# Kernel tuning notes

Hardware: AMD Instinct MI355X
Metric: run time of the kernel (lower is better)

## Reference

```python
import jax, jax.numpy as jnp
import numpy as np

SCALE = 0.5
DROP_P = 0.2

def setup_inputs() -> dict:
    key = jax.random.key(0)
    k1, k2 = jax.random.split(key)
    x1 = jax.random.normal(k1, (8, 2048, 128), dtype=jnp.float32)
    x2 = jax.random.normal(k2, (8, 2048, 128), dtype=jnp.float32)
    return {"x1": x1, "x2": x2}

def reference(x1, x2):
    # scores: [B, M, N] = x1 @ x2^T, scaled by 0.5
    scores = jnp.einsum('bmd,bnd->bmn', x1, x2) * SCALE
    probs = jax.nn.softmax(scores, axis=-1)
    # dropout p=0.2 (training mode in the torch source); fixed key for determinism
    keep = jax.random.bernoulli(jax.random.key(42), 1.0 - DROP_P, probs.shape)
    probs = jnp.where(keep, probs / (1.0 - DROP_P), 0.0)
    # out: [B, M, D] = probs @ x2
    return jnp.einsum('bmn,bnd->bmd', probs, x2)
```

## Files before the change

### kernel.cpp

```cpp
#include <hip/hip_runtime.h>
#include <stdint.h>


typedef __bf16 bf16x8 __attribute__((ext_vector_type(8)));
typedef float f32x4 __attribute__((ext_vector_type(4)));

union FragAB {
  bf16x8 v;
  uint32_t u[4];
};

__device__ __forceinline__ uint32_t rotl32(uint32_t x, uint32_t r) {
  return (x << r) | (x >> (32u - r));
}

__device__ __forceinline__ void threefry2x32_k42(uint32_t in0, uint32_t in1,
                                                 uint32_t& o0, uint32_t& o1) {
  const uint32_t ks0 = 0u;
  const uint32_t ks1 = 42u;
  const uint32_t ks2 = 0x1BD11BDAu ^ 0u ^ 42u;
  uint32_t x0 = in0 + ks0;
  uint32_t x1 = in1 + ks1;
#define TFR(r) { x0 += x1; x1 = rotl32(x1, r); x1 ^= x0; }
  TFR(13u) TFR(15u) TFR(26u) TFR(6u)
  x0 += ks1; x1 += ks2 + 1u;
  TFR(17u) TFR(29u) TFR(16u) TFR(24u)
  x0 += ks2; x1 += ks0 + 2u;
  TFR(13u) TFR(15u) TFR(26u) TFR(6u)
  x0 += ks0; x1 += ks1 + 3u;
  TFR(17u) TFR(29u) TFR(16u) TFR(24u)
  x0 += ks1; x1 += ks2 + 4u;
  TFR(13u) TFR(15u) TFR(26u) TFR(6u)
  x0 += ks2; x1 += ks0 + 5u;
#undef TFR
  o0 = x0; o1 = x1;
}

__device__ __forceinline__ uint32_t pack_bf16(float a, float b) {
  __bf16 ba = (__bf16)a;
  __bf16 bb = (__bf16)b;
  uint32_t ua = (uint32_t)__builtin_bit_cast(uint16_t, ba);
  uint32_t ub = (uint32_t)__builtin_bit_cast(uint16_t, bb);
  return ua | (ub << 16);
}

#define KEEP_LT 3435974144u
#define MBIAS 40.0f

__launch_bounds__(256, 4)
__global__ void prep_kernel(const float* __restrict__ x2,
                            uint4* __restrict__ KF,
                            uint4* __restrict__ VF) {
  const int tid = threadIdx.x;
  const int w = tid >> 6;
  const int lane = tid & 63;
  const int l15 = lane & 15;
  const int g = lane >> 4;
  const int T = blockIdx.x;
  const int b = blockIdx.y;
  const float* xb = x2 + (size_t)b * 2048 * 128;

  #pragma unroll
  for (int h = 0; h < 2; ++h) {
    const int n = T * 32 + h * 16 + l15;
    const float* p = xb + (size_t)n * 128 + w * 32 + 8 * g;
    float4 f0 = *(const float4*)(p);
    float4 f1 = *(const float4*)(p + 4);
    uint4 u;
    u.x = pack_bf16(f0.x, f0.y);
    u.y = pack_bf16(f0.z, f0.w);
    u.z = pack_bf16(f1.x, f1.y);
    u.w = pack_bf16(f1.z, f1.w);
    KF[(size_t)((b * 64 + T) * 8 + w * 2 + h) * 64 + lane] = u;
  }

  #pragma unroll
  for (int i = 0; i < 2; ++i) {
    const int dt = w + 4 * i;
    const int d = dt * 16 + l15;
    const float* p = xb + (size_t)(T * 32 + 8 * g) * 128 + d;
    uint4 u;
    u.x = pack_bf16(p[0],   p[128]);
    u.y = pack_bf16(p[256], p[384]);
    u.z = pack_bf16(p[512], p[640]);
    u.w = pack_bf16(p[768], p[896]);
    VF[(size_t)((b * 64 + T) * 8 + dt) * 64 + lane] = u;
  }
}

__launch_bounds__(256, 4)
__global__ void attn2_kernel(const float* __restrict__ x1,
                             const uint4* __restrict__ KF,
                             const uint4* __restrict__ VF,
                             float* __restrict__ out) {
  __shared__ __attribute__((aligned(16))) uint32_t SMEM[8768];

  const int tid = threadIdx.x;
  const int w = __builtin_amdgcn_readfirstlane(tid >> 6);
  const int lane = tid & 63;
  const int l15 = lane & 15;
  const int g = lane >> 4;
  const int b = blockIdx.y;
  const int m0 = blockIdx.x * 16;

  uint32_t* PbW = &SMEM[w * 320];

  const float QSCALE = 0.5f * 1.44269504088896340736f;
  FragAB qf[4];
  {
    const float* qp_base = x1 + ((size_t)b * 2048 + m0 + l15) * 128;
    #pragma unroll
    for (int c = 0; c < 4; ++c) {
      const float* qp = qp_base + c * 32 + g * 8;
      float4 f0 = *(const float4*)(qp);
      float4 f1 = *(const float4*)(qp + 4);
      qf[c].u[0] = pack_bf16(f0.x * QSCALE, f0.y * QSCALE);
      qf[c].u[1] = pack_bf16(f0.z * QSCALE, f0.w * QSCALE);
      qf[c].u[2] = pack_bf16(f1.x * QSCALE, f1.y * QSCALE);
      qf[c].u[3] = pack_bf16(f1.z * QSCALE, f1.w * QSCALE);
    }
  }

  f32x4 o[8];
  #pragma unroll
  for (int dt = 0; dt < 8; ++dt) o[dt] = (f32x4){0.f, 0.f, 0.f, 0.f};
  float lsum = 0.f;

  const uint32_t rb = (uint32_t)b * 4194304u +
                      (uint32_t)(m0 + l15) * 2048u + (uint32_t)(w * 512);

  const uint4* kfp = KF + (size_t)((b * 64 + w * 16) * 8) * 64 + lane;
  const uint4* vfp = VF + (size_t)((b * 64 + w * 16) * 8) * 64 + lane;

  for (int tile = 0; tile < 16; ++tile) {
    f32x4 sa[2];
    sa[0] = (f32x4){0.f, 0.f, 0.f, 0.f};
    sa[1] = (f32x4){0.f, 0.f, 0.f, 0.f};
    #pragma unroll
    for (int c = 0; c < 4; ++c) {
      uint4 a0 = kfp[(c * 2 + 0) * 64];
      uint4 a1 = kfp[(c * 2 + 1) * 64];
      FragAB k0, k1;
      k0.u[0] = a0.x; k0.u[1] = a0.y; k0.u[2] = a0.z; k0.u[3] = a0.w;
      k1.u[0] = a1.x; k1.u[1] = a1.y; k1.u[2] = a1.z; k1.u[3] = a1.w;
      sa[0] = __builtin_amdgcn_mfma_f32_16x16x32_bf16(k0.v, qf[c].v, sa[0], 0, 0, 0);
      sa[1] = __builtin_amdgcn_mfma_f32_16x16x32_bf16(k1.v, qf[c].v, sa[1], 0, 0, 0);
    }

    #pragma unroll
    for (int t = 0; t < 2; ++t) {
      float p0 = __builtin_amdgcn_exp2f(sa[t][0] - MBIAS);
      float p1 = __builtin_amdgcn_exp2f(sa[t][1] - MBIAS);
      float p2 = __builtin_amdgcn_exp2f(sa[t][2] - MBIAS);
      float p3 = __builtin_amdgcn_exp2f(sa[t][3] - MBIAS);
      lsum += (p0 + p1) + (p2 + p3);
      uint32_t ib = rb + (uint32_t)(tile * 32 + t * 16 + 4 * g);
      uint32_t h0, h1, bits;
      threefry2x32_k42(0u, ib + 0u, h0, h1); bits = h0 ^ h1;
      float q0 = (bits < KEEP_LT) ? p0 : 0.0f;
      threefry2x32_k42(0u, ib + 1u, h0, h1); bits = h0 ^ h1;
      float q1 = (bits < KEEP_LT) ? p1 : 0.0f;
      threefry2x32_k42(0u, ib + 2u, h0, h1); bits = h0 ^ h1;
      float q2 = (bits < KEEP_LT) ? p2 : 0.0f;
      threefry2x32_k42(0u, ib + 3u, h0, h1); bits = h0 ^ h1;
      float q3 = (bits < KEEP_LT) ? p3 : 0.0f;
      *(uint2*)&PbW[l15 * 20 + t * 8 + 2 * g] =
          make_uint2(pack_bf16(q0, q1), pack_bf16(q2, q3));
    }
    asm volatile("s_waitcnt lgkmcnt(0)" ::: "memory");
    FragAB pa;
    {
      uint4 pu = *(const uint4*)&PbW[l15 * 20 + 4 * g];
      pa.u[0] = pu.x; pa.u[1] = pu.y; pa.u[2] = pu.z; pa.u[3] = pu.w;
    }

    #pragma unroll
    for (int dt = 0; dt < 8; ++dt) {
      uint4 vv = vfp[dt * 64];
      FragAB vb;
      vb.u[0] = vv.x; vb.u[1] = vv.y; vb.u[2] = vv.z; vb.u[3] = vv.w;
      o[dt] = __builtin_amdgcn_mfma_f32_16x16x32_bf16(pa.v, vb.v, o[dt], 0, 0, 0);
    }
    kfp += 512;
    vfp += 512;
  }

  __syncthreads();
  float* EP = (float*)&SMEM[0];
  float* EPL = EP + 8192;
  EPL[l15 * 36 + w * 4 + g] = lsum;
  #pragma unroll
  for (int dt = 0; dt < 8; ++dt)
    #pragma unroll
    for (int r = 0; r < 4; ++r)
      EP[((w * 8 + dt) * 4 + r) * 64 + lane] = o[dt][r];
  __syncthreads();
  float scale[4];
  #pragma unroll
  for (int r = 0; r < 4; ++r) {
    const float4* lp = (const float4*)&EPL[(4 * g + r) * 36];
    float4 A = lp[0], B4 = lp[1], C4 = lp[2], D4 = lp[3];
    float L = ((A.x + A.y) + (A.z + A.w)) + ((B4.x + B4.y) + (B4.z + B4.w)) +
              ((C4.x + C4.y) + (C4.z + C4.w)) + ((D4.x + D4.y) + (D4.z + D4.w));
    scale[r] = 1.0f / (L * 0.8f);
  }
  #pragma unroll
  for (int i = 0; i < 2; ++i) {
    const int dt = w * 2 + i;
    #pragma unroll
    for (int r = 0; r < 4; ++r) {
      int base = (dt * 4 + r) * 64 + lane;
      float tot = EP[base] + EP[base + 2048] + EP[base + 4096] + EP[base + 6144];
      out[((size_t)b * 2048 + m0 + 4 * g + r) * 128 + dt * 16 + l15] =
          tot * scale[r];
    }
  }
}

__launch_bounds__(256, 2)
__global__ void attn_kernel(const float* __restrict__ x1,
                            const float* __restrict__ x2,
                            float* __restrict__ out) {
  __shared__ __attribute__((aligned(16))) uint32_t SMEM[4][4800];

  const int tid = threadIdx.x;
  const int wv = __builtin_amdgcn_readfirstlane(tid >> 6);
  const int lane = tid & 63;
  const int l15 = lane & 15;
  const int g = lane >> 4;
  const int b = blockIdx.y;
  const int m0 = blockIdx.x * 32;

  uint32_t* KtW = &SMEM[wv][0];
  uint32_t* VtW = &SMEM[wv][2176];
  uint32_t* PbW = &SMEM[wv][4480];

  const float QSCALE = 0.5f * 1.44269504088896340736f;
  FragAB qf[2][4];
  #pragma unroll
  for (int s = 0; s < 2; ++s) {
    const float* qp_base = x1 + ((size_t)b * 2048 + m0 + s * 16 + l15) * 128;
    #pragma unroll
    for (int c = 0; c < 4; ++c) {
      const float* qp = qp_base + c * 32 + g * 8;
      float4 f0 = *(const float4*)(qp);
      float4 f1 = *(const float4*)(qp + 4);
      qf[s][c].u[0] = pack_bf16(f0.x * QSCALE, f0.y * QSCALE);
      qf[s][c].u[1] = pack_bf16(f0.z * QSCALE, f0.w * QSCALE);
      qf[s][c].u[2] = pack_bf16(f1.x * QSCALE, f1.y * QSCALE);
      qf[s][c].u[3] = pack_bf16(f1.z * QSCALE, f1.w * QSCALE);
    }
  }

  f32x4 o[2][8];
  #pragma unroll
  for (int s = 0; s < 2; ++s)
    #pragma unroll
    for (int dt = 0; dt < 8; ++dt) o[s][dt] = (f32x4){0.f, 0.f, 0.f, 0.f};
  float lsum[2] = {0.f, 0.f};

  uint32_t rb[2];
  #pragma unroll
  for (int s = 0; s < 2; ++s)
    rb[s] = (uint32_t)b * 4194304u +
            (uint32_t)(m0 + s * 16 + l15) * 2048u + (uint32_t)(wv * 512);

  const float4* x2b4 = (const float4*)(x2 + (size_t)b * 2048 * 128);
  const uint32_t permsel = (l15 & 1) ? 0x07060302u : 0x05040100u;

  for (int tile = 0; tile < 16; ++tile) {
    const int n0g = wv * 512 + tile * 32;

    #pragma unroll
    for (int i = 0; i < 16; ++i) {
      int n = 2 * i + (lane >> 5);
      int dq = lane & 31;
      float4 v = x2b4[(size_t)(n0g + n) * 32 + dq];
      uint32_t p0 = pack_bf16(v.x, v.y);
      uint32_t p1 = pack_bf16(v.z, v.w);
      *(uint2*)&KtW[n * 68 + 2 * dq] = make_uint2(p0, p1);
      VtW[dq * 36 + n] = p0;
      VtW[(dq + 32) * 36 + n] = p1;
    }
    asm volatile("s_waitcnt lgkmcnt(0)" ::: "memory");

    f32x4 sa[2][2];
    #pragma unroll
    for (int s = 0; s < 2; ++s)
      #pragma unroll
      for (int t = 0; t < 2; ++t) sa[s][t] = (f32x4){0.f, 0.f, 0.f, 0.f};
    #pragma unroll
    for (int c = 0; c < 4; ++c) {
      FragAB k0, k1;
      uint4 a0 = *(const uint4*)&KtW[l15 * 68 + c * 16 + 4 * g];
      uint4 a1 = *(const uint4*)&KtW[(16 + l15) * 68 + c * 16 + 4 * g];
      k0.u[0] = a0.x; k0.u[1] = a0.y; k0.u[2] = a0.z; k0.u[3] = a0.w;
      k1.u[0] = a1.x; k1.u[1] = a1.y; k1.u[2] = a1.z; k1.u[3] = a1.w;
      sa[0][0] = __builtin_amdgcn_mfma_f32_16x16x32_bf16(k0.v, qf[0][c].v, sa[0][0], 0, 0, 0);
      sa[0][1] = __builtin_amdgcn_mfma_f32_16x16x32_bf16(k1.v, qf[0][c].v, sa[0][1], 0, 0, 0);
      sa[1][0] = __builtin_amdgcn_mfma_f32_16x16x32_bf16(k0.v, qf[1][c].v, sa[1][0], 0, 0, 0);
      sa[1][1] = __builtin_amdgcn_mfma_f32_16x16x32_bf16(k1.v, qf[1][c].v, sa[1][1], 0, 0, 0);
    }

    FragAB pa[2];
    #pragma unroll
    for (int s = 0; s < 2; ++s) {
      #pragma unroll
      for (int t = 0; t < 2; ++t) {
        float p0 = __builtin_amdgcn_exp2f(sa[s][t][0] - MBIAS);
        float p1 = __builtin_amdgcn_exp2f(sa[s][t][1] - MBIAS);
        float p2 = __builtin_amdgcn_exp2f(sa[s][t][2] - MBIAS);
        float p3 = __builtin_amdgcn_exp2f(sa[s][t][3] - MBIAS);
        lsum[s] += (p0 + p1) + (p2 + p3);
        uint32_t ib = rb[s] + (uint32_t)(tile * 32 + t * 16 + 4 * g);
        uint32_t h0, h1, bits;
        threefry2x32_k42(0u, ib + 0u, h0, h1); bits = h0 ^ h1;
        float q0 = (bits < KEEP_LT) ? p0 : 0.0f;
        threefry2x32_k42(0u, ib + 1u, h0, h1); bits = h0 ^ h1;
        float q1 = (bits < KEEP_LT) ? p1 : 0.0f;
        threefry2x32_k42(0u, ib + 2u, h0, h1); bits = h0 ^ h1;
        float q2 = (bits < KEEP_LT) ? p2 : 0.0f;
        threefry2x32_k42(0u, ib + 3u, h0, h1); bits = h0 ^ h1;
        float q3 = (bits < KEEP_LT) ? p3 : 0.0f;
        *(uint2*)&PbW[l15 * 20 + t * 8 + 2 * g] =
            make_uint2(pack_bf16(q0, q1), pack_bf16(q2, q3));
      }
      asm volatile("s_waitcnt lgkmcnt(0)" ::: "memory");
      uint4 pu = *(const uint4*)&PbW[l15 * 20 + 4 * g];
      pa[s].u[0] = pu.x; pa[s].u[1] = pu.y; pa[s].u[2] = pu.z; pa[s].u[3] = pu.w;
    }

    #pragma unroll
    for (int dt = 0; dt < 8; ++dt) {
      int rowp = ((l15 >> 1) & 1) * 32 + 4 * dt + (l15 >> 2);
      const uint32_t* vr = &VtW[rowp * 36 + 8 * g];
      uint4 U0 = *(const uint4*)vr;
      uint4 U1 = *(const uint4*)(vr + 4);
      FragAB vb;
      vb.u[0] = __builtin_amdgcn_perm(U0.y, U0.x, permsel);
      vb.u[1] = __builtin_amdgcn_perm(U0.w, U0.z, permsel);
      vb.u[2] = __builtin_amdgcn_perm(U1.y, U1.x, permsel);
      vb.u[3] = __builtin_amdgcn_perm(U1.w, U1.z, permsel);
      o[0][dt] = __builtin_amdgcn_mfma_f32_16x16x32_bf16(pa[0].v, vb.v, o[0][dt], 0, 0, 0);
      o[1][dt] = __builtin_amdgcn_mfma_f32_16x16x32_bf16(pa[1].v, vb.v, o[1][dt], 0, 0, 0);
    }
  }

  __syncthreads();
  float* EP = (float*)&SMEM[0][0];
  #pragma unroll
  for (int s = 0; s < 2; ++s) {
    #pragma unroll
    for (int dt = 0; dt < 8; ++dt)
      #pragma unroll
      for (int r = 0; r < 4; ++r)
        EP[(((wv * 2 + s) * 8 + dt) * 4 + r) * 64 + lane] = o[s][dt][r];
    EP[16384 + (s * 16 + l15) * 16 + wv * 4 + g] = lsum[s];
  }
  __syncthreads();
  const int s = wv >> 1;
  float scale[4];
  #pragma unroll
  for (int r = 0; r < 4; ++r) {
    const float4* lp = (const float4*)&EP[16384 + (s * 16 + 4 * g + r) * 16];
    float4 A = lp[0], B4 = lp[1], C4 = lp[2], D4 = lp[3];
    float L = ((A.x + A.y) + (A.z + A.w)) + ((B4.x + B4.y) + (B4.z + B4.w)) +
              ((C4.x + C4.y) + (C4.z + C4.w)) + ((D4.x + D4.y) + (D4.z + D4.w));
    scale[r] = 1.0f / (L * 0.8f);
  }
  #pragma unroll
  for (int it = 0; it < 4; ++it) {
    int dt = (wv * 4 + it) & 7;
    #pragma unroll
    for (int r = 0; r < 4; ++r) {
      int base = ((s * 8 + dt) * 4 + r) * 64 + lane;
      float tot = EP[base] + EP[base + 4096] + EP[base + 8192] + EP[base + 12288];
      out[((size_t)b * 2048 + m0 + s * 16 + 4 * g + r) * 128 + dt * 16 + l15] =
          tot * scale[r];
    }
  }
}

extern "C" void kernel_launch(void* const* d_in, const int* in_sizes, int n_in,
                              void* d_out, int out_size, void* d_ws, size_t ws_size,
                              hipStream_t stream) {
  const float* x1 = (const float*)d_in[0];
  const float* x2 = (const float*)d_in[1];
  float* out = (float*)d_out;
  if (d_ws != nullptr && ws_size >= (size_t)8 * 1024 * 1024) {
    uint4* KF = (uint4*)d_ws;
    uint4* VF = KF + 262144;
    prep_kernel<<<dim3(64, 8, 1), dim3(256, 1, 1), 0, stream>>>(x2, KF, VF);
    attn2_kernel<<<dim3(128, 8, 1), dim3(256, 1, 1), 0, stream>>>(x1, KF, VF, out);
  } else {
    attn_kernel<<<dim3(64, 8, 1), dim3(256, 1, 1), 0, stream>>>(x1, x2, out);
  }
}
```

Measured before the change: 146.1 us.

## Use 512-thread blocks sharing K/V tiles across two query halves

Replaces the 256-thread attention kernel with a 512-thread version where two groups of four waves handle two 16-row query slices that read the same K/V chunks. A per-tile barrier keeps them in lockstep so the shared K/V loads can hit in cache. Other changes: Q fragments now live in LDS instead of registers, block IDs are remapped so batch varies fastest, MFMA sections are wrapped in s_setprio, and the MBIAS subtraction before exp2 is dropped. Risks are the per-tile barrier stalls, extra LDS reads for Q, and possible exp overflow without the bias.

```diff
diff --git a/kernel.cpp b/kernel.cpp
--- a/kernel.cpp
+++ b/kernel.cpp
@@ -4,11 +4,6 @@
 
 typedef __bf16 bf16x8 __attribute__((ext_vector_type(8)));
 typedef float f32x4 __attribute__((ext_vector_type(4)));
-
-union FragAB {
-  bf16x8 v;
-  uint32_t u[4];
-};
 
 __device__ __forceinline__ uint32_t rotl32(uint32_t x, uint32_t r) {
   return (x << r) | (x >> (32u - r));
@@ -88,73 +83,83 @@
   }
 }
 
-__launch_bounds__(256, 4)
-__global__ void attn2_kernel(const float* __restrict__ x1,
+__launch_bounds__(512, 4)
+__global__ void attn6_kernel(const float* __restrict__ x1,
                              const uint4* __restrict__ KF,
                              const uint4* __restrict__ VF,
                              float* __restrict__ out) {
-  __shared__ __attribute__((aligned(16))) uint32_t SMEM[8768];
+  __shared__ __attribute__((aligned(16))) uint32_t SMEM[8832];
 
   const int tid = threadIdx.x;
   const int w = __builtin_amdgcn_readfirstlane(tid >> 6);
   const int lane = tid & 63;
   const int l15 = lane & 15;
   const int g = lane >> 4;
-  const int b = blockIdx.y;
-  const int m0 = blockIdx.x * 16;
-
-  uint32_t* PbW = &SMEM[w * 320];
+  const int q = w & 3;
+  const int hs = w >> 2;
+  const int id = blockIdx.y * 64 + blockIdx.x;
+  const int b = id & 7;
+  const int mt = id >> 3;
+  const int m0 = mt * 32;
+
+  uint32_t* Qld = &SMEM[0];
+  uint32_t* PbW = &SMEM[2048 + w * 320];
 
   const float QSCALE = 0.5f * 1.44269504088896340736f;
-  FragAB qf[4];
-  {
-    const float* qp_base = x1 + ((size_t)b * 2048 + m0 + l15) * 128;
+  if (q == 0) {
+    const float* qp_base =
+        x1 + ((size_t)b * 2048 + m0 + hs * 16 + l15) * 128;
     #pragma unroll
     for (int c = 0; c < 4; ++c) {
       const float* qp = qp_base + c * 32 + g * 8;
       float4 f0 = *(const float4*)(qp);
       float4 f1 = *(const float4*)(qp + 4);
-      qf[c].u[0] = pack_bf16(f0.x * QSCALE, f0.y * QSCALE);
-      qf[c].u[1] = pack_bf16(f0.z * QSCALE, f0.w * QSCALE);
-      qf[c].u[2] = pack_bf16(f1.x * QSCALE, f1.y * QSCALE);
-      qf[c].u[3] = pack_bf16(f1.z * QSCALE, f1.w * QSCALE);
-    }
-  }
+      uint4 u;
+      u.x = pack_bf16(f0.x * QSCALE, f0.y * QSCALE);
+      u.y = pack_bf16(f0.z * QSCALE, f0.w * QSCALE);
+      u.z = pack_bf16(f1.x * QSCALE, f1.y * QSCALE);
+      u.w = pack_bf16(f1.z * QSCALE, f1.w * QSCALE);
+      *(uint4*)&Qld[hs * 1024 + (c * 64 + lane) * 4] = u;
+    }
+  }
+  __syncthreads();
 
   f32x4 o[8];
   #pragma unroll
   for (int dt = 0; dt < 8; ++dt) o[dt] = (f32x4){0.f, 0.f, 0.f, 0.f};
   float lsum = 0.f;
 
-  const uint32_t rb = (uint32_t)b * 4194304u +
-                      (uint32_t)(m0 + l15) * 2048u + (uint32_t)(w * 512);
-
-  const uint4* kfp = KF + (size_t)((b * 64 + w * 16) * 8) * 64 + lane;
-  const uint4* vfp = VF + (size_t)((b * 64 + w * 16) * 8) * 64 + lane;
+  const uint32_t rbg = (uint32_t)b * 4194304u +
+                       (uint32_t)(m0 + hs * 16 + l15) * 2048u +
+                       (uint32_t)(q * 512) + (uint32_t)(4 * g);
+
+  const uint4* kfp = KF + (size_t)((b * 64 + q * 16) * 8) * 64 + lane;
+  const uint4* vfp = VF + (size_t)((b * 64 + q * 16) * 8) * 64 + lane;
 
   for (int tile = 0; tile < 16; ++tile) {
     f32x4 sa[2];
     sa[0] = (f32x4){0.f, 0.f, 0.f, 0.f};
     sa[1] = (f32x4){0.f, 0.f, 0.f, 0.f};
+    __builtin_amdgcn_s_setprio(1);
     #pragma unroll
     for (int c = 0; c < 4; ++c) {
-      uint4 a0 = kfp[(c * 2 + 0) * 64];
-      uint4 a1 = kfp[(c * 2 + 1) * 64];
-      FragAB k0, k1;
-      k0.u[0] = a0.x; k0.u[1] = a0.y; k0.u[2] = a0.z; k0.u[3] = a0.w;
-      k1.u[0] = a1.x; k1.u[1] = a1.y; k1.u[2] = a1.z; k1.u[3] = a1.w;
-      sa[0] = __builtin_amdgcn_mfma_f32_16x16x32_bf16(k0.v, qf[c].v, sa[0], 0, 0, 0);
-      sa[1] = __builtin_amdgcn_mfma_f32_16x16x32_bf16(k1.v, qf[c].v, sa[1], 0, 0, 0);
-    }
+      bf16x8 qc = __builtin_bit_cast(
+          bf16x8, *(const uint4*)&Qld[hs * 1024 + (c * 64 + lane) * 4]);
+      bf16x8 k0 = __builtin_bit_cast(bf16x8, kfp[(c * 2 + 0) * 64]);
+      bf16x8 k1 = __builtin_bit_cast(bf16x8, kfp[(c * 2 + 1) * 64]);
+      sa[0] = __builtin_amdgcn_mfma_f32_16x16x32_bf16(k0, qc, sa[0], 0, 0, 0);
+      sa[1] = __builtin_amdgcn_mfma_f32_16x16x32_bf16(k1, qc, sa[1], 0, 0, 0);
+    }
+    __builtin_amdgcn_s_setprio(0);
 
     #pragma unroll
     for (int t = 0; t < 2; ++t) {
-      float p0 = __builtin_amdgcn_exp2f(sa[t][0] - MBIAS);
-      float p1 = __builtin_amdgcn_exp2f(sa[t][1] - MBIAS);
-      float p2 = __builtin_amdgcn_exp2f(sa[t][2] - MBIAS);
-      float p3 = __builtin_amdgcn_exp2f(sa[t][3] - MBIAS);
+      float p0 = __builtin_amdgcn_exp2f(sa[t][0]);
+      float p1 = __builtin_amdgcn_exp2f(sa[t][1]);
+      float p2 = __builtin_amdgcn_exp2f(sa[t][2]);
+      float p3 = __builtin_amdgcn_exp2f(sa[t][3]);
       lsum += (p0 + p1) + (p2 + p3);
-      uint32_t ib = rb + (uint32_t)(tile * 32 + t * 16 + 4 * g);
+      const uint32_t ib = rbg + (uint32_t)(tile * 32 + t * 16);
       uint32_t h0, h1, bits;
       threefry2x32_k42(0u, ib + 0u, h0, h1); bits = h0 ^ h1;
       float q0 = (bits < KEEP_LT) ? p0 : 0.0f;
@@ -168,54 +173,59 @@
           make_uint2(pack_bf16(q0, q1), pack_bf16(q2, q3));
     }
     asm volatile("s_waitcnt lgkmcnt(0)" ::: "memory");
-    FragAB pa;
-    {
-      uint4 pu = *(const uint4*)&PbW[l15 * 20 + 4 * g];
-      pa.u[0] = pu.x; pa.u[1] = pu.y; pa.u[2] = pu.z; pa.u[3] = pu.w;
-    }
-
+    uint4 pu = *(const uint4*)&PbW[l15 * 20 + 4 * g];
+    bf16x8 pav = __builtin_bit_cast(bf16x8, pu);
+
+    __builtin_amdgcn_s_setprio(1);
     #pragma unroll
     for (int dt = 0; dt < 8; ++dt) {
-      uint4 vv = vfp[dt * 64];
-      FragAB vb;
-      vb.u[0] = vv.x; vb.u[1] = vv.y; vb.u[2] = vv.z; vb.u[3] = vv.w;
-      o[dt] = __builtin_amdgcn_mfma_f32_16x16x32_bf16(pa.v, vb.v, o[dt], 0, 0, 0);
-    }
+      bf16x8 vb = __builtin_bit_cast(bf16x8, vfp[dt * 64]);
+      o[dt] = __builtin_amdgcn_mfma_f32_16x16x32_bf16(pav, vb, o[dt], 0, 0, 0);
+    }
+    __builtin_amdgcn_s_setprio(0);
+
     kfp += 512;
     vfp += 512;
-  }
-
-  __syncthreads();
+    __syncthreads();
+  }
+
   float* EP = (float*)&SMEM[0];
   float* EPL = EP + 8192;
-  EPL[l15 * 36 + w * 4 + g] = lsum;
-  #pragma unroll
-  for (int dt = 0; dt < 8; ++dt)
-    #pragma unroll
-    for (int r = 0; r < 4; ++r)
-      EP[((w * 8 + dt) * 4 + r) * 64 + lane] = o[dt][r];
-  __syncthreads();
-  float scale[4];
-  #pragma unroll
-  for (int r = 0; r < 4; ++r) {
-    const float4* lp = (const float4*)&EPL[(4 * g + r) * 36];
-    float4 A = lp[0], B4 = lp[1], C4 = lp[2], D4 = lp[3];
-    float L = ((A.x + A.y) + (A.z + A.w)) + ((B4.x + B4.y) + (B4.z + B4.w)) +
-              ((C4.x + C4.y) + (C4.z + C4.w)) + ((D4.x + D4.y) + (D4.z + D4.w));
-    scale[r] = 1.0f / (L * 0.8f);
-  }
-  #pragma unroll
-  for (int i = 0; i < 2; ++i) {
-    const int dt = w * 2 + i;
+  #pragma unroll
+  for (int pass = 0; pass < 2; ++pass) {
+    if (pass == 1) __syncthreads();
+    if (hs == pass) {
+      EPL[l15 * 36 + q * 4 + g] = lsum;
+      #pragma unroll
+      for (int dt = 0; dt < 8; ++dt)
+        #pragma unroll
+        for (int r = 0; r < 4; ++r)
+          EP[((q * 8 + dt) * 4 + r) * 64 + lane] = o[dt][r];
+    }
+    __syncthreads();
+    float scale[4];
     #pragma unroll
     for (int r = 0; r < 4; ++r) {
-      int base = (dt * 4 + r) * 64 + lane;
+      const float4* lp = (const float4*)&EPL[(4 * g + r) * 36];
+      float4 A = lp[0], B4 = lp[1], C4 = lp[2], D4 = lp[3];
+      float L = ((A.x + A.y) + (A.z + A.w)) + ((B4.x + B4.y) + (B4.z + B4.w)) +
+                ((C4.x + C4.y) + (C4.z + C4.w)) + ((D4.x + D4.y) + (D4.z + D4.w));
+      scale[r] = 1.0f / (L * 0.8f);
+    }
+    #pragma unroll
+    for (int r = 0; r < 4; ++r) {
+      const int base = (w * 4 + r) * 64 + lane;
       float tot = EP[base] + EP[base + 2048] + EP[base + 4096] + EP[base + 6144];
-      out[((size_t)b * 2048 + m0 + 4 * g + r) * 128 + dt * 16 + l15] =
+      out[((size_t)b * 2048 + m0 + pass * 16 + 4 * g + r) * 128 + w * 16 + l15] =
           tot * scale[r];
     }
   }
 }
+
+union FragAB {
+  bf16x8 v;
+  uint32_t u[4];
+};
 
 __launch_bounds__(256, 2)
 __global__ void attn_kernel(const float* __restrict__ x1,
@@ -391,7 +401,7 @@
     uint4* KF = (uint4*)d_ws;
     uint4* VF = KF + 262144;
     prep_kernel<<<dim3(64, 8, 1), dim3(256, 1, 1), 0, stream>>>(x2, KF, VF);
-    attn2_kernel<<<dim3(128, 8, 1), dim3(256, 1, 1), 0, stream>>>(x1, KF, VF, out);
+    attn6_kernel<<<dim3(64, 8, 1), dim3(512, 1, 1), 0, stream>>>(x1, KF, VF, out);
   } else {
     attn_kernel<<<dim3(64, 8, 1), dim3(256, 1, 1), 0, stream>>>(x1, x2, out);
   }
```

Result: slower. 174.6 us (+19.5%).
